# Optimization experiments

Hardware: AMD Instinct MI355X
Metric: run time of the kernel (lower is better)

The kernel has to match this reference:

```python
import jax, jax.numpy as jnp
import numpy as np

L, DIRS, H, I, B, T = 2, 2, 512, 1024, 64, 1024


def _gru_dir(x_seq, h0, w_ih, w_hh, b_ih, b_hh, reverse):
    """Run one GRU direction. x_seq: (B,T,in), h0: (B,H). Returns (out (B,T,H), h_T (B,H))."""
    # Precompute input projections for all timesteps: (T,B,3H)
    gi = jnp.einsum('bti,gi->tbg', x_seq, w_ih) + b_ih

    def step(h, gi_t):
        gh = h @ w_hh.T + b_hh                      # (B,3H)
        i_r, i_z, i_n = jnp.split(gi_t, 3, axis=-1)
        h_r, h_z, h_n = jnp.split(gh, 3, axis=-1)
        r = jax.nn.sigmoid(i_r + h_r)
        z = jax.nn.sigmoid(i_z + h_z)
        n = jnp.tanh(i_n + r * h_n)
        h_new = (1.0 - z) * n + z * h
        return h_new, h_new

    h_T, out = jax.lax.scan(step, h0, gi, reverse=reverse)
    return out.transpose(1, 0, 2), h_T            # (B,T,H), (B,H)


def setup_inputs() -> dict:
    key = jax.random.key(0)
    ks = jax.random.split(key, 6)
    s = 1.0 / np.sqrt(H)  # PyTorch-style init scale, avoids gate saturation
    return {
        'x':    jax.random.normal(ks[0], (B, T, I), jnp.float32),
        'h0':   jax.random.normal(ks[1], (L * DIRS, B, H), jnp.float32) * s,
        'w_ih': jax.random.normal(ks[2], (L, DIRS, 3 * H, I), jnp.float32) * s,
        'w_hh': jax.random.normal(ks[3], (L, DIRS, 3 * H, H), jnp.float32) * s,
        'b_ih': jax.random.normal(ks[4], (L, DIRS, 3 * H), jnp.float32) * s,
        'b_hh': jax.random.normal(ks[5], (L, DIRS, 3 * H), jnp.float32) * s,
    }


def reference(x, h0, w_ih, w_hh, b_ih, b_hh):
    layer_in = x
    h_finals = []
    for l in range(L):  # small fixed loop over structurally distinct layers
        out_f, hT_f = _gru_dir(layer_in, h0[2 * l],     w_ih[l, 0], w_hh[l, 0], b_ih[l, 0], b_hh[l, 0], reverse=False)
        out_b, hT_b = _gru_dir(layer_in, h0[2 * l + 1], w_ih[l, 1], w_hh[l, 1], b_ih[l, 1], b_hh[l, 1], reverse=True)
        layer_in = jnp.concatenate([out_f, out_b], axis=-1)  # (B,T,2H)
        h_finals.extend([hT_f, hT_b])
    h_n = jnp.stack(h_finals, axis=0)  # (L*2, B, H), PyTorch ordering
    return layer_in, h_n
```

## Files before the change

### kernel.cpp

```cpp
#include <hip/hip_runtime.h>
#include <stdint.h>
#include <stdio.h>

#define TL 1024
#define BB 64
#define HH 512
#define II 1024
#define NL 2
#define BT_ (BB*TL)
#define G3_ 1536
#define N2_ 3072

typedef _Float16 h8 __attribute__((ext_vector_type(8)));
typedef _Float16 h4 __attribute__((ext_vector_type(4)));
typedef _Float16 h2 __attribute__((ext_vector_type(2)));
typedef float    f4 __attribute__((ext_vector_type(4)));
typedef unsigned int u4 __attribute__((ext_vector_type(4)));
typedef unsigned int u2v __attribute__((ext_vector_type(2)));

__global__ void cvt_f2h(const float* __restrict__ src, _Float16* __restrict__ dst, size_t n4) {
  size_t i = (size_t)blockIdx.x*blockDim.x + threadIdx.x;
  size_t stride = (size_t)gridDim.x*blockDim.x;
  for (; i < n4; i += stride) {
    f4 v = ((const f4*)src)[i];
    h4 o;
    o[0] = (_Float16)v[0]; o[1] = (_Float16)v[1];
    o[2] = (_Float16)v[2]; o[3] = (_Float16)v[3];
    ((h4*)dst)[i] = o;
  }
}

#define LDA 40
__launch_bounds__(256)
__global__ void gemm_gi(const _Float16* __restrict__ A, const _Float16* __restrict__ Bw,
                        const float* __restrict__ bias, _Float16* __restrict__ gi)
{
  const int bn = blockIdx.x, bm = blockIdx.y;
  const int tid = threadIdx.x;
  const int wave = tid >> 6, lane = tid & 63;
  const int wm = wave >> 1, wn = wave & 1;
  const int lo = lane & 15, hi = lane >> 4;
  __shared__ _Float16 As[128*LDA];
  __shared__ _Float16 Bs[128*LDA];
  f4 acc[4][4] = {};
  const int r0 = tid >> 2, c0 = (tid & 3)*8;
  const _Float16* Ag = A + (size_t)(bm*128)*II;
  const _Float16* Bg = Bw + (size_t)(bn*128)*II;
  u4 a0 = *(const u4*)(Ag + (size_t)r0*II + c0);
  u4 a1 = *(const u4*)(Ag + (size_t)(64+r0)*II + c0);
  u4 b0 = *(const u4*)(Bg + (size_t)r0*II + c0);
  u4 b1 = *(const u4*)(Bg + (size_t)(64+r0)*II + c0);
  for (int kt = 0; kt < 32; ++kt) {
    __syncthreads();
    *(u4*)&As[r0*LDA + c0] = a0;
    *(u4*)&As[(64+r0)*LDA + c0] = a1;
    *(u4*)&Bs[r0*LDA + c0] = b0;
    *(u4*)&Bs[(64+r0)*LDA + c0] = b1;
    if (kt+1 < 32) {
      const int off = (kt+1)*32 + c0;
      a0 = *(const u4*)(Ag + (size_t)r0*II + off);
      a1 = *(const u4*)(Ag + (size_t)(64+r0)*II + off);
      b0 = *(const u4*)(Bg + (size_t)r0*II + off);
      b1 = *(const u4*)(Bg + (size_t)(64+r0)*II + off);
    }
    __syncthreads();
    h8 af[4], bf[4];
    #pragma unroll
    for (int i = 0; i < 4; ++i)
      af[i] = *(const h8*)&As[(wm*64 + i*16 + lo)*LDA + hi*8];
    #pragma unroll
    for (int j = 0; j < 4; ++j)
      bf[j] = *(const h8*)&Bs[(wn*64 + j*16 + lo)*LDA + hi*8];
    #pragma unroll
    for (int i = 0; i < 4; ++i)
      #pragma unroll
      for (int j = 0; j < 4; ++j)
        acc[i][j] = __builtin_amdgcn_mfma_f32_16x16x32_f16(af[i], bf[j], acc[i][j], 0, 0, 0);
  }
  const int nbase = bn*128 + wn*64;
  const int mbase = bm*128 + wm*64;
  #pragma unroll
  for (int j = 0; j < 4; ++j) {
    int n = nbase + j*16 + lo;
    int dir = (n >= G3_) ? 1 : 0;
    int row = n - dir*G3_;
    float bs = bias[n];
    #pragma unroll
    for (int i = 0; i < 4; ++i) {
      int m0 = mbase + i*16 + hi*4;
      #pragma unroll
      for (int v = 0; v < 4; ++v)
        gi[((size_t)dir*BT_ + (size_t)(m0+v))*G3_ + row] = (_Float16)(acc[i][j][v] + bs);
    }
  }
}

#define LDW 520
__launch_bounds__(384, 1)
__global__ void gru_layer(const _Float16* __restrict__ gi,
                          const _Float16* __restrict__ whh,
                          const float* __restrict__ bhh,
                          const float* __restrict__ h0,
                          unsigned long long* __restrict__ tagh,
                          _Float16* __restrict__ out_mid,
                          float* __restrict__ out_fin,
                          float* __restrict__ hn_out,
                          int layer)
{
  const int bid = blockIdx.x;
  const int gg = bid & 7, d = gg & 1, g = gg >> 1;
  const int member = bid >> 3;
  const int j0 = member * 32, b0 = g * 16;
  const int tid = threadIdx.x;
  const int wave = tid >> 6, lane = tid & 63, lo = lane & 15, hi = lane >> 4;
  const int gate = wave >> 1, jh = wave & 1;

  __shared__ _Float16 wlds[3][32][LDW];
  __shared__ _Float16 hlds[16][LDW];
  __shared__ float    ghlds[3][32][17];

  const _Float16* wsrc = whh + (size_t)d*G3_*HH;
  #pragma unroll
  for (int it = 0; it < 16; ++it) {
    int idx = it*384 + tid;
    int row = idx >> 6;
    int c8 = (idx & 63) * 8;
    int gt = row >> 5, jj = row & 31;
    u4 v = *(const u4*)(wsrc + (size_t)(gt*HH + j0 + jj)*HH + c8);
    *(u4*)&wlds[gt][jj][c8] = v;
  }

  const int ejp = tid & 15;
  const int eb  = tid >> 4;
  const bool ew = (tid < 256);
  const int ejA = j0 + 2*ejp;

  unsigned long long* Tb = tagh + (size_t)d*2*BB*256;

  float hj[2];
  float bhr[2], bhz[2], bhn[2];

  if (ew) {
    #pragma unroll
    for (int u = 0; u < 2; ++u) {
      bhr[u] = bhh[(size_t)d*G3_ + 0*HH + ejA + u];
      bhz[u] = bhh[(size_t)d*G3_ + 1*HH + ejA + u];
      bhn[u] = bhh[(size_t)d*G3_ + 2*HH + ejA + u];
      hj[u]  = h0[((size_t)(2*layer + d)*BB + b0 + eb)*HH + ejA + u];
    }
    h2 p; p[0] = (_Float16)hj[0]; p[1] = (_Float16)hj[1];
    unsigned long long ent = (unsigned long long)__builtin_bit_cast(unsigned, p) | (1ull << 32);
    unsigned long long* ptr = Tb + (size_t)0*BB*256 + (size_t)(b0 + eb)*256 + (member*16 + ejp);
    __hip_atomic_store(ptr, ent, __ATOMIC_RELAXED, __HIP_MEMORY_SCOPE_AGENT);
  }
  __syncthreads();

  for (int s = 0; s < TL; ++s) {
    const int t = d ? (TL-1 - s) : s;
    const int rpar = s & 1, wpar = rpar ^ 1;
    const unsigned tgt = (unsigned)(s + 1);
    const unsigned long long* Trd = Tb + (size_t)rpar*BB*256;
    unsigned giR = 0, giZ = 0, giN = 0;
    unsigned long long E[16];
    if (ew) {
      const _Float16* p = gi + ((size_t)d*BT_ + (size_t)(b0 + eb)*TL + t)*(size_t)G3_ + ejA;
      giR = *(const unsigned*)(p);
      giZ = *(const unsigned*)(p + HH);
      giN = *(const unsigned*)(p + 2*HH);
      #pragma unroll
      for (int q = 0; q < 4; ++q)
        #pragma unroll
        for (int k = 0; k < 4; ++k) {
          int i = tid*2 + (k >> 1);
          E[q*4+k] = __hip_atomic_load(
              Trd + (size_t)(b0 + (i >> 5))*256 + q*64 + (i & 31)*2 + (k & 1),
              __ATOMIC_RELAXED, __HIP_MEMORY_SCOPE_AGENT);
        }
    }
    f4 acc = {0.f, 0.f, 0.f, 0.f};
    #pragma unroll
    for (int q = 0; q < 4; ++q) {
      if (ew) {
        for (;;) {
          unsigned ok = 1u;
          #pragma unroll
          for (int k = 0; k < 4; ++k)
            ok &= (unsigned)((E[q*4+k] >> 32) >= tgt);
          if (ok) break;
          #pragma unroll
          for (int k = 0; k < 4; ++k) {
            int i = tid*2 + (k >> 1);
            E[q*4+k] = __hip_atomic_load(
                Trd + (size_t)(b0 + (i >> 5))*256 + q*64 + (i & 31)*2 + (k & 1),
                __ATOMIC_RELAXED, __HIP_MEMORY_SCOPE_AGENT);
          }
        }
        #pragma unroll
        for (int k = 0; k < 2; ++k) {
          int i = tid*2 + k;
          int b = i >> 5, p = i & 31;
          u2v dv; dv[0] = (unsigned)E[q*4 + k*2]; dv[1] = (unsigned)E[q*4 + k*2 + 1];
          *(u2v*)&hlds[b][q*128 + p*4] = dv;
        }
      }
      asm volatile("s_waitcnt lgkmcnt(0)" ::: "memory");
      __builtin_amdgcn_s_barrier();
      __builtin_amdgcn_sched_barrier(0);
      #pragma unroll
      for (int kk = q*4; kk < q*4 + 4; ++kk) {
        h8 af = *(const h8*)&hlds[lo][kk*32 + hi*8];
        h8 bf = *(const h8*)&wlds[gate][jh*16 + lo][kk*32 + hi*8];
        acc = __builtin_amdgcn_mfma_f32_16x16x32_f16(af, bf, acc, 0, 0, 0);
      }
    }
    #pragma unroll
    for (int v = 0; v < 4; ++v)
      ghlds[gate][jh*16 + lo][hi*4 + v] = acc[v];
    __syncthreads();
    if (ew) {
      h2 pR = __builtin_bit_cast(h2, giR);
      h2 pZ = __builtin_bit_cast(h2, giZ);
      h2 pN = __builtin_bit_cast(h2, giN);
      h2 hnew; float hv[2];
      #pragma unroll
      for (int u = 0; u < 2; ++u) {
        float ir = (float)pR[u], iz = (float)pZ[u], inn = (float)pN[u];
        float hr = ghlds[0][2*ejp+u][eb] + bhr[u];
        float hz = ghlds[1][2*ejp+u][eb] + bhz[u];
        float hn = ghlds[2][2*ejp+u][eb] + bhn[u];
        float rr = 1.f/(1.f + __expf(-(ir + hr)));
        float zz = 1.f/(1.f + __expf(-(iz + hz)));
        float xx = inn + rr*hn;
        float nn = 1.f - 2.f/(__expf(2.f*xx) + 1.f);
        float h  = (1.f - zz)*nn + zz*hj[u];
        hj[u] = h; hnew[u] = (_Float16)h; hv[u] = h;
      }
      unsigned hu = __builtin_bit_cast(unsigned, hnew);
      unsigned long long ent = (unsigned long long)hu | ((unsigned long long)(s + 2) << 32);
      unsigned long long* ptr = Tb + (size_t)wpar*BB*256 + (size_t)(b0 + eb)*256 + (member*16 + ejp);
      __hip_atomic_store(ptr, ent, __ATOMIC_RELAXED, __HIP_MEMORY_SCOPE_AGENT);
      if (out_mid) {
        *(unsigned*)(out_mid + ((size_t)(b0+eb)*TL + t)*(size_t)(2*HH) + d*HH + ejA) = hu;
      } else {
        u2v ov; ov[0] = __builtin_bit_cast(unsigned, hv[0]); ov[1] = __builtin_bit_cast(unsigned, hv[1]);
        *(u2v*)(out_fin + ((size_t)(b0+eb)*TL + t)*(size_t)(2*HH) + d*HH + ejA) = ov;
      }
    }
  }
  if (ew) {
    #pragma unroll
    for (int u = 0; u < 2; ++u)
      hn_out[((size_t)(2*layer + d)*BB + b0 + eb)*HH + ejA + u] = hj[u];
  }
}

extern "C" void kernel_launch(void* const* d_in, const int* in_sizes, int n_in,
                              void* d_out, int out_size, void* d_ws, size_t ws_size,
                              hipStream_t stream) {
  (void)in_sizes; (void)n_in; (void)out_size;
  const float* x   = (const float*)d_in[0];
  const float* h0  = (const float*)d_in[1];
  const float* wih = (const float*)d_in[2];
  const float* whh = (const float*)d_in[3];
  const float* bih = (const float*)d_in[4];
  const float* bhh = (const float*)d_in[5];
  float* out = (float*)d_out;

  char* ws = (char*)d_ws;
  size_t off = 0;
  auto alloc = [&](size_t bytes) {
    char* p = ws + off;
    off += (bytes + 255) & ~(size_t)255;
    return p;
  };
  _Float16* x16   = (_Float16*)alloc((size_t)BT_*II*2);
  _Float16* mid16 = (_Float16*)alloc((size_t)BT_*II*2);
  _Float16* gi16  = (_Float16*)alloc((size_t)2*BT_*G3_*2);
  _Float16* wih16 = (_Float16*)alloc((size_t)NL*N2_*II*2);
  _Float16* whh16 = (_Float16*)alloc((size_t)NL*N2_*HH*2);
  unsigned long long* tagh = (unsigned long long*)alloc((size_t)NL*2*2*BB*256*8);
  if (off > ws_size) {
    fprintf(stderr, "kernel_launch: workspace too small: need %zu have %zu\n", off, ws_size);
    return;
  }

  hipMemsetAsync(tagh, 0, (size_t)NL*2*2*BB*256*8, stream);
  cvt_f2h<<<2048, 256, 0, stream>>>(x,   x16,   (size_t)BT_*II/4);
  cvt_f2h<<<512,  256, 0, stream>>>(wih, wih16, (size_t)NL*N2_*II/4);
  cvt_f2h<<<512,  256, 0, stream>>>(whh, whh16, (size_t)NL*N2_*HH/4);

  float* hn = out + (size_t)BT_*II;

  gemm_gi<<<dim3(24, 512), 256, 0, stream>>>(x16, wih16, bih, gi16);
  gru_layer<<<128, 384, 0, stream>>>(gi16, whh16, bhh, h0, tagh,
                                     mid16, nullptr, hn, 0);
  gemm_gi<<<dim3(24, 512), 256, 0, stream>>>(mid16, wih16 + (size_t)N2_*II, bih + N2_, gi16);
  gru_layer<<<128, 384, 0, stream>>>(gi16, whh16 + (size_t)N2_*HH, bhh + N2_, h0,
                                     tagh + (size_t)2*2*BB*256, nullptr, out, hn, 1);
}
```

Before: 7.194 ms.

## Add producer waves to prefetch next-step input gates into LDS

Result: slower. 8.177 ms (+13.7%).

```diff
diff --git a/kernel.cpp b/kernel.cpp
--- a/kernel.cpp
+++ b/kernel.cpp
@@ -96,7 +96,7 @@
 }
 
 #define LDW 520
-__launch_bounds__(384, 1)
+__launch_bounds__(512, 1)
 __global__ void gru_layer(const _Float16* __restrict__ gi,
                           const _Float16* __restrict__ whh,
                           const float* __restrict__ bhh,
@@ -118,11 +118,12 @@
   __shared__ _Float16 wlds[3][32][LDW];
   __shared__ _Float16 hlds[16][LDW];
   __shared__ float    ghlds[3][32][17];
+  __shared__ _Float16 gil[2][16][3][32];
 
   const _Float16* wsrc = whh + (size_t)d*G3_*HH;
   #pragma unroll
-  for (int it = 0; it < 16; ++it) {
-    int idx = it*384 + tid;
+  for (int it = 0; it < 12; ++it) {
+    int idx = it*512 + tid;
     int row = idx >> 6;
     int c8 = (idx & 63) * 8;
     int gt = row >> 5, jj = row & 31;
@@ -139,6 +140,7 @@
 
   float hj[2];
   float bhr[2], bhz[2], bhn[2];
+  unsigned long long E[16];
 
   if (ew) {
     #pragma unroll
@@ -152,6 +154,30 @@
     unsigned long long ent = (unsigned long long)__builtin_bit_cast(unsigned, p) | (1ull << 32);
     unsigned long long* ptr = Tb + (size_t)0*BB*256 + (size_t)(b0 + eb)*256 + (member*16 + ejp);
     __hip_atomic_store(ptr, ent, __ATOMIC_RELAXED, __HIP_MEMORY_SCOPE_AGENT);
+    const unsigned long long* Trd = Tb;
+    #pragma unroll
+    for (int q = 0; q < 4; ++q)
+      #pragma unroll
+      for (int k = 0; k < 4; ++k) {
+        int i = tid*2 + (k >> 1);
+        E[q*4+k] = __hip_atomic_load(
+            Trd + (size_t)(b0 + (i >> 5))*256 + q*64 + (i & 31)*2 + (k & 1),
+            __ATOMIC_RELAXED, __HIP_MEMORY_SCOPE_AGENT);
+      }
+  }
+  if (wave >= 6) {
+    const int t0 = d ? (TL-1) : 0;
+    const int L = tid - 384;
+    #pragma unroll
+    for (int r = 0; r < 2; ++r) {
+      int idx = L + r*128;
+      if (idx < 192) {
+        int seg = idx >> 2, q = idx & 3;
+        int gt = seg >> 4, b = seg & 15;
+        u4 v = *(const u4*)(gi + (size_t)d*BT_*G3_ + ((size_t)(b0+b)*TL + t0)*G3_ + gt*HH + j0 + q*8);
+        *(u4*)&gil[0][b][gt][q*8] = v;
+      }
+    }
   }
   __syncthreads();
 
@@ -160,91 +186,132 @@
     const int rpar = s & 1, wpar = rpar ^ 1;
     const unsigned tgt = (unsigned)(s + 1);
     const unsigned long long* Trd = Tb + (size_t)rpar*BB*256;
-    unsigned giR = 0, giZ = 0, giN = 0;
-    unsigned long long E[16];
-    if (ew) {
-      const _Float16* p = gi + ((size_t)d*BT_ + (size_t)(b0 + eb)*TL + t)*(size_t)G3_ + ejA;
-      giR = *(const unsigned*)(p);
-      giZ = *(const unsigned*)(p + HH);
-      giN = *(const unsigned*)(p + 2*HH);
-      #pragma unroll
-      for (int q = 0; q < 4; ++q)
-        #pragma unroll
-        for (int k = 0; k < 4; ++k) {
-          int i = tid*2 + (k >> 1);
-          E[q*4+k] = __hip_atomic_load(
-              Trd + (size_t)(b0 + (i >> 5))*256 + q*64 + (i & 31)*2 + (k & 1),
-              __ATOMIC_RELAXED, __HIP_MEMORY_SCOPE_AGENT);
-        }
-    }
-    f4 acc = {0.f, 0.f, 0.f, 0.f};
-    #pragma unroll
-    for (int q = 0; q < 4; ++q) {
+
+    if (wave < 6) {
       if (ew) {
         for (;;) {
           unsigned ok = 1u;
           #pragma unroll
-          for (int k = 0; k < 4; ++k)
-            ok &= (unsigned)((E[q*4+k] >> 32) >= tgt);
+          for (int k = 0; k < 16; ++k)
+            ok &= (unsigned)((E[k] >> 32) >= tgt);
           if (ok) break;
+          #pragma unroll
+          for (int q = 0; q < 4; ++q)
+            #pragma unroll
+            for (int k = 0; k < 4; ++k) {
+              int i = tid*2 + (k >> 1);
+              E[q*4+k] = __hip_atomic_load(
+                  Trd + (size_t)(b0 + (i >> 5))*256 + q*64 + (i & 31)*2 + (k & 1),
+                  __ATOMIC_RELAXED, __HIP_MEMORY_SCOPE_AGENT);
+            }
+        }
+        #pragma unroll
+        for (int q = 0; q < 4; ++q)
+          #pragma unroll
+          for (int k = 0; k < 2; ++k) {
+            int i = tid*2 + k;
+            int b = i >> 5, p = i & 31;
+            u2v dv; dv[0] = (unsigned)E[q*4 + k*2]; dv[1] = (unsigned)E[q*4 + k*2 + 1];
+            *(u2v*)&hlds[b][q*128 + p*4] = dv;
+          }
+      }
+      asm volatile("s_waitcnt lgkmcnt(0)" ::: "memory");
+      __builtin_amdgcn_s_barrier();
+      __builtin_amdgcn_sched_barrier(0);
+      f4 acc = {0.f, 0.f, 0.f, 0.f};
+      #pragma unroll
+      for (int kk = 0; kk < 16; ++kk) {
+        h8 af = *(const h8*)&hlds[lo][kk*32 + hi*8];
+        h8 bf = *(const h8*)&wlds[gate][jh*16 + lo][kk*32 + hi*8];
+        acc = __builtin_amdgcn_mfma_f32_16x16x32_f16(af, bf, acc, 0, 0, 0);
+      }
+      #pragma unroll
+      for (int v = 0; v < 4; ++v)
+        ghlds[gate][jh*16 + lo][hi*4 + v] = acc[v];
+      asm volatile("s_waitcnt lgkmcnt(0)" ::: "memory");
+      __builtin_amdgcn_s_barrier();
+      __builtin_amdgcn_sched_barrier(0);
+      if (ew) {
+        unsigned giR = *(const unsigned*)&gil[rpar][eb][0][2*ejp];
+        unsigned giZ = *(const unsigned*)&gil[rpar][eb][1][2*ejp];
+        unsigned giN = *(const unsigned*)&gil[rpar][eb][2][2*ejp];
+        h2 pR = __builtin_bit_cast(h2, giR);
+        h2 pZ = __builtin_bit_cast(h2, giZ);
+        h2 pN = __builtin_bit_cast(h2, giN);
+        h2 hnew; float hv[2];
+        #pragma unroll
+        for (int u = 0; u < 2; ++u) {
+          float ir = (float)pR[u], iz = (float)pZ[u], inn = (float)pN[u];
+          float hr = ghlds[0][2*ejp+u][eb] + bhr[u];
+          float hz = ghlds[1][2*ejp+u][eb] + bhz[u];
+          float hn = ghlds[2][2*ejp+u][eb] + bhn[u];
+          float rr = 1.f/(1.f + __expf(-(ir + hr)));
+          float zz = 1.f/(1.f + __expf(-(iz + hz)));
+          float xx = inn + rr*hn;
+          float nn = 1.f - 2.f/(__expf(2.f*xx) + 1.f);
+          float h  = (1.f - zz)*nn + zz*hj[u];
+          hj[u] = h; hnew[u] = (_Float16)h; hv[u] = h;
+        }
+        unsigned hu = __builtin_bit_cast(unsigned, hnew);
+        unsigned long long ent = (unsigned long long)hu | ((unsigned long long)(s + 2) << 32);
+        unsigned long long* ptr = Tb + (size_t)wpar*BB*256 + (size_t)(b0 + eb)*256 + (member*16 + ejp);
+        __hip_atomic_store(ptr, ent, __ATOMIC_RELAXED, __HIP_MEMORY_SCOPE_AGENT);
+        if (out_mid) {
+          *(unsigned*)(out_mid + ((size_t)(b0+eb)*TL + t)*(size_t)(2*HH) + d*HH + ejA) = hu;
+        } else {
+          u2v ov; ov[0] = __builtin_bit_cast(unsigned, hv[0]); ov[1] = __builtin_bit_cast(unsigned, hv[1]);
+          *(u2v*)(out_fin + ((size_t)(b0+eb)*TL + t)*(size_t)(2*HH) + d*HH + ejA) = ov;
+        }
+        const unsigned long long* Trn = Tb + (size_t)wpar*BB*256;
+        #pragma unroll
+        for (int q = 0; q < 4; ++q)
           #pragma unroll
           for (int k = 0; k < 4; ++k) {
             int i = tid*2 + (k >> 1);
             E[q*4+k] = __hip_atomic_load(
-                Trd + (size_t)(b0 + (i >> 5))*256 + q*64 + (i & 31)*2 + (k & 1),
+                Trn + (size_t)(b0 + (i >> 5))*256 + q*64 + (i & 31)*2 + (k & 1),
                 __ATOMIC_RELAXED, __HIP_MEMORY_SCOPE_AGENT);
           }
-        }
-        #pragma unroll
-        for (int k = 0; k < 2; ++k) {
-          int i = tid*2 + k;
-          int b = i >> 5, p = i & 31;
-          u2v dv; dv[0] = (unsigned)E[q*4 + k*2]; dv[1] = (unsigned)E[q*4 + k*2 + 1];
-          *(u2v*)&hlds[b][q*128 + p*4] = dv;
+      }
+    } else {
+      const int L = tid - 384;
+      u4 va = {}, vb = {};
+      int have = 0;
+      if (s + 1 < TL) {
+        const int tn = d ? (TL-1 - (s+1)) : (s+1);
+        const _Float16* gbase = gi + (size_t)d*BT_*G3_ + (size_t)0;
+        {
+          int idx = L;
+          int seg = idx >> 2, q = idx & 3;
+          int gt = seg >> 4, b = seg & 15;
+          va = *(const u4*)(gbase + ((size_t)(b0+b)*TL + tn)*G3_ + gt*HH + j0 + q*8);
+        }
+        if (L < 64) {
+          int idx = L + 128;
+          int seg = idx >> 2, q = idx & 3;
+          int gt = seg >> 4, b = seg & 15;
+          vb = *(const u4*)(gbase + ((size_t)(b0+b)*TL + tn)*G3_ + gt*HH + j0 + q*8);
+        }
+        have = 1;
+      }
+      __builtin_amdgcn_s_barrier();
+      if (have) {
+        const int wbuf = wpar;
+        {
+          int idx = L;
+          int seg = idx >> 2, q = idx & 3;
+          int gt = seg >> 4, b = seg & 15;
+          *(u4*)&gil[wbuf][b][gt][q*8] = va;
+        }
+        if (L < 64) {
+          int idx = L + 128;
+          int seg = idx >> 2, q = idx & 3;
+          int gt = seg >> 4, b = seg & 15;
+          *(u4*)&gil[wbuf][b][gt][q*8] = vb;
         }
       }
       asm volatile("s_waitcnt lgkmcnt(0)" ::: "memory");
       __builtin_amdgcn_s_barrier();
-      __builtin_amdgcn_sched_barrier(0);
-      #pragma unroll
-      for (int kk = q*4; kk < q*4 + 4; ++kk) {
-        h8 af = *(const h8*)&hlds[lo][kk*32 + hi*8];
-        h8 bf = *(const h8*)&wlds[gate][jh*16 + lo][kk*32 + hi*8];
-        acc = __builtin_amdgcn_mfma_f32_16x16x32_f16(af, bf, acc, 0, 0, 0);
-      }
-    }
-    #pragma unroll
-    for (int v = 0; v < 4; ++v)
-      ghlds[gate][jh*16 + lo][hi*4 + v] = acc[v];
-    __syncthreads();
-    if (ew) {
-      h2 pR = __builtin_bit_cast(h2, giR);
-      h2 pZ = __builtin_bit_cast(h2, giZ);
-      h2 pN = __builtin_bit_cast(h2, giN);
-      h2 hnew; float hv[2];
-      #pragma unroll
-      for (int u = 0; u < 2; ++u) {
-        float ir = (float)pR[u], iz = (float)pZ[u], inn = (float)pN[u];
-        float hr = ghlds[0][2*ejp+u][eb] + bhr[u];
-        float hz = ghlds[1][2*ejp+u][eb] + bhz[u];
-        float hn = ghlds[2][2*ejp+u][eb] + bhn[u];
-        float rr = 1.f/(1.f + __expf(-(ir + hr)));
-        float zz = 1.f/(1.f + __expf(-(iz + hz)));
-        float xx = inn + rr*hn;
-        float nn = 1.f - 2.f/(__expf(2.f*xx) + 1.f);
-        float h  = (1.f - zz)*nn + zz*hj[u];
-        hj[u] = h; hnew[u] = (_Float16)h; hv[u] = h;
-      }
-      unsigned hu = __builtin_bit_cast(unsigned, hnew);
-      unsigned long long ent = (unsigned long long)hu | ((unsigned long long)(s + 2) << 32);
-      unsigned long long* ptr = Tb + (size_t)wpar*BB*256 + (size_t)(b0 + eb)*256 + (member*16 + ejp);
-      __hip_atomic_store(ptr, ent, __ATOMIC_RELAXED, __HIP_MEMORY_SCOPE_AGENT);
-      if (out_mid) {
-        *(unsigned*)(out_mid + ((size_t)(b0+eb)*TL + t)*(size_t)(2*HH) + d*HH + ejA) = hu;
-      } else {
-        u2v ov; ov[0] = __builtin_bit_cast(unsigned, hv[0]); ov[1] = __builtin_bit_cast(unsigned, hv[1]);
-        *(u2v*)(out_fin + ((size_t)(b0+eb)*TL + t)*(size_t)(2*HH) + d*HH + ejA) = ov;
-      }
     }
   }
   if (ew) {
@@ -292,9 +359,9 @@
   float* hn = out + (size_t)BT_*II;
 
   gemm_gi<<<dim3(24, 512), 256, 0, stream>>>(x16, wih16, bih, gi16);
-  gru_layer<<<128, 384, 0, stream>>>(gi16, whh16, bhh, h0, tagh,
+  gru_layer<<<128, 512, 0, stream>>>(gi16, whh16, bhh, h0, tagh,
                                      mid16, nullptr, hn, 0);
   gemm_gi<<<dim3(24, 512), 256, 0, stream>>>(mid16, wih16 + (size_t)N2_*II, bih + N2_, gi16);
-  gru_layer<<<128, 384, 0, stream>>>(gi16, whh16 + (size_t)N2_*HH, bhh + N2_, h0,
+  gru_layer<<<128, 512, 0, stream>>>(gi16, whh16 + (size_t)N2_*HH, bhh + N2_, h0,
                                      tagh + (size_t)2*2*BB*256, nullptr, out, hn, 1);
 }
```
